# Kernel tuning notes

Hardware: AMD Instinct MI355X
Metric: run time of the kernel (lower is better)

## Reference

```python
import jax, jax.numpy as jnp
import numpy as np

K = 3          # kernel_size
PAD = 1        # padding
FOCAL = 50.0
DMIN = 1.0
DMAX = 50.0
ORIG_H = 512.0  # original_image_size[1]


def setup_inputs() -> dict:
    key = jax.random.key(0)
    k1, k2 = jax.random.split(key)
    x = jax.random.normal(k1, (4, 64, 256, 256), dtype=jnp.float32)
    # conv weight [out_ch, in_ch, K, K] (bias=False)
    W = jax.random.normal(k2, (64, 64, K, K), dtype=jnp.float32) * 0.05
    return {"x": x, "W": W}


def _bilinear(img, xs, ys):
    """Bilinear sample img [B,C,H,W] at float pixel coords xs, ys [B,Ho,Wo].
    Zero padding outside the image (grid_sample semantics)."""
    B, C, H, Wd = img.shape
    Ho, Wo = xs.shape[1], xs.shape[2]
    x0 = jnp.floor(xs); y0 = jnp.floor(ys)
    wx1 = xs - x0; wx0 = 1.0 - wx1
    wy1 = ys - y0; wy0 = 1.0 - wy1
    img_flat = img.reshape(B, C, H * Wd)

    def gat(ix, iy):
        ixi = ix.astype(jnp.int32); iyi = iy.astype(jnp.int32)
        valid = (ixi >= 0) & (ixi < Wd) & (iyi >= 0) & (iyi < H)
        idx = jnp.clip(iyi, 0, H - 1) * Wd + jnp.clip(ixi, 0, Wd - 1)
        v = jnp.take_along_axis(img_flat, idx.reshape(B, 1, Ho * Wo), axis=2)
        v = v.reshape(B, C, Ho, Wo)
        return v * valid[:, None].astype(img.dtype)

    return (gat(x0, y0) * (wx0 * wy0)[:, None]
            + gat(x0 + 1, y0) * (wx1 * wy0)[:, None]
            + gat(x0, y0 + 1) * (wx0 * wy1)[:, None]
            + gat(x0 + 1, y0 + 1) * (wx1 * wy1)[:, None])


def reference(x, W):
    B, C, H, Wd = x.shape
    downsample = ORIG_H / H  # 2.0 for H=256

    # upper branch: plain 3x3 conv, padding 1, no bias
    x_upper = jax.lax.conv_general_dilated(x, W, (1, 1), [(PAD, PAD), (PAD, PAD)])

    # geometry -> clamped depth (geometry_method='max', formulation='depth')
    depth = jnp.clip(jnp.max(x, axis=1), DMIN, DMAX)  # [B,H,W]

    # Frontal homography: Hom01 = I with [1,2] = focal/(downsample*depth);
    # its inverse Hom10 shifts y by -s.
    s = FOCAL / (downsample * depth)  # [B,H,W]

    xi = jnp.arange(Wd, dtype=x.dtype)[None, None, :]
    yi = jnp.arange(H, dtype=x.dtype)[None, :, None]
    xs = jnp.broadcast_to(xi, (B, H, Wd))
    ys = yi - s  # Hom10 applied to pixel coords

    # warp input with per-pixel Hom10 (pass_warped_images=True)
    x2 = _bilinear(x, xs, ys)

    # deformable conv: per-pixel offset from Hom10 is (dx,dy)=(0,-s) for all 9 taps
    x_lower = jnp.zeros_like(x_upper)
    for ky in range(K):
        for kx in range(K):
            sx = xs + (kx - PAD)
            sy = ys + (ky - PAD)
            tap = _bilinear(x2, sx, sy)  # [B,C,H,W]
            x_lower = x_lower + jnp.einsum('bchw,oc->bohw', tap, W[:, :, ky, kx])

    # project with 'min' over the stacked (upper, lower) branches
    return jnp.minimum(x_upper, x_lower)
```

## Files before the change

### kernel.cpp

```cpp
#include <hip/hip_runtime.h>
#include <cmath>

constexpr int BB = 4, CC = 64, HH = 256, WW = 256;
constexpr int WP = 258;
constexpr int C2R = 257;

typedef short short8 __attribute__((ext_vector_type(8)));
typedef float f32x4 __attribute__((ext_vector_type(4)));
#define MFMA_BF16 __builtin_amdgcn_mfma_f32_16x16x32_bf16

typedef __attribute__((address_space(1))) const unsigned gptr_t;
typedef __attribute__((address_space(3))) unsigned lptr_t;

union U16x8 { uint4 v; unsigned short h[8]; };
union U16x4 { uint2 v; unsigned short h[4]; };

__device__ inline unsigned short f2bf(float f) {
  unsigned u = __builtin_bit_cast(unsigned, f);
  u += 0x7fffu + ((u >> 16) & 1u);
  return (unsigned short)(u >> 16);
}
__device__ inline unsigned short f2bf_trunc(float f) {
  return (unsigned short)(__builtin_bit_cast(unsigned, f) >> 16);
}
__device__ inline float bf2f(unsigned short h) {
  unsigned u = ((unsigned)h) << 16;
  return __builtin_bit_cast(float, u);
}

__global__ __launch_bounds__(256, 4) void k_pack(const float* __restrict__ x,
                                                 const float* __restrict__ Wt,
                                                 float* __restrict__ s,
                                                 unsigned short* __restrict__ xn,
                                                 unsigned short* __restrict__ Wp) {
  __shared__ float tile[CC * 129];
  __shared__ float pmax[2][128];
  const int t = threadIdx.x;
  const int half = blockIdx.x & 1, y = blockIdx.x >> 1, b = blockIdx.y;
  const int px0 = half * 128;
  const int pxl = t & 127, chb = (t >> 7) * 32;

  if (b == 0 && blockIdx.x < 18) {
    int gid = blockIdx.x * 256 + t;
    int lane = gid & 63, kc = (gid >> 6) & 1, mt = (gid >> 7) & 3, tap = gid >> 9;
    int o = mt * 16 + (lane & 15);
    int kb = kc * 32 + (lane >> 4) * 8;
    int ky = tap / 3, kx = tap % 3;
    U16x8 r;
#pragma unroll
    for (int j = 0; j < 8; ++j)
      r.h[j] = f2bf(Wt[o * 576 + (kb + j) * 9 + ky * 3 + kx]);
    ((uint4*)Wp)[gid] = r.v;
  }

  const float* base = x + (size_t)b * CC * HH * WW + (size_t)y * WW + px0 + pxl;
  float m = -1e30f;
#pragma unroll 8
  for (int i = 0; i < 32; ++i) {
    float v = base[(size_t)(chb + i) * HH * WW];
    tile[(chb + i) * 129 + pxl] = v;
    m = fmaxf(m, v);
  }
  pmax[t >> 7][pxl] = m;

  uint4* xn4 = (uint4*)xn;
  if (t < 8) {
    int col = half ? (WP - 1) : 0;
    xn4[(((size_t)(b * HH + y) * WP + col) * CC + t * 8) >> 3] =
        make_uint4(0, 0, 0, 0);
  }
  __syncthreads();

  if (t < 128) {
    float mm = fmaxf(pmax[0][t], pmax[1][t]);
    s[(b * HH + y) * WW + px0 + t] = 25.0f / fminf(fmaxf(mm, 1.0f), 50.0f);
  }
#pragma unroll
  for (int g = 0; g < 4; ++g) {
    int px = g * 32 + (t >> 3), c8 = t & 7;
    U16x8 r;
#pragma unroll
    for (int j = 0; j < 8; ++j) r.h[j] = f2bf(tile[(c8 * 8 + j) * 129 + px]);
    xn4[(((size_t)(b * HH + y) * WP + px0 + px + 1) * CC + c8 * 8) >> 3] = r.v;
  }
}

__global__ __launch_bounds__(256, 4) void k_lower(const unsigned short* __restrict__ xn,
                                                  const unsigned short* __restrict__ Wp,
                                                  const float* __restrict__ s,
                                                  unsigned short* __restrict__ c2) {
  __shared__ uint4 lds[2112];
  const int t = threadIdx.x;
  const int ctile = blockIdx.x & 3, tr = blockIdx.x >> 2;
  const int b = blockIdx.y;
  const int r0 = tr * 2 - 1;
  const int colBase = ctile * 64;

  const uint4* xn4 = (const uint4*)xn;

  float sva[9];
#pragma unroll
  for (int j = 0; j < 9; ++j) {
    int idx = j * 256 + t;
    bool act = (j < 8) || (t < 64);
    int rr_ = idx / 528, rem = idx % 528;
    int col_ = rem >> 3;
    int xrow = r0 - 1 + rr_;
    bool va = act && (xrow >= 0) && (xrow < HH);
    int pxc = min(max(colBase + col_ - 1, 0), WW - 1);
    sva[j] = va ? s[(b * HH + min(max(xrow, 0), HH - 1)) * WW + pxc] : 0.0f;
  }

#pragma unroll
  for (int h = 0; h < 2; ++h) {
    const int jb = h * 5;
    const int n = h ? 4 : 5;
    uint4 u0[5], u1[5];
    float w0a[5], w1a[5];
    int la[5];
    bool act[5], va[5];
#pragma unroll
    for (int j = 0; j < 5; ++j) {
      if (j >= n) break;
      const int e = jb + j;
      int idx = e * 256 + t;
      act[j] = (e < 8) || (t < 64);
      int rr_ = idx / 528, rem = idx % 528;
      int col_ = rem >> 3, ch_ = rem & 7;
      int xrow = r0 - 1 + rr_;
      va[j] = act[j] && (xrow >= 0) && (xrow < HH);
      la[j] = (rr_ * 66 + col_) * 8 + (ch_ ^ (col_ & 7));
      float ys = (float)xrow - sva[e];
      float fy = floorf(ys);
      float wfr = ys - fy;
      int i0 = (int)fy;
      w0a[j] = (i0 >= 0) ? 1.0f - wfr : 0.0f;
      w1a[j] = (i0 + 1 >= 0) ? wfr : 0.0f;
      int a0 = min(max(i0, 0), HH - 1), a1 = min(max(i0 + 1, 0), HH - 1);
      int o0 = ((b * HH + a0) * WP + colBase + col_) * 8 + ch_;
      int o1 = ((b * HH + a1) * WP + colBase + col_) * 8 + ch_;
      if (va[j]) {
        u0[j] = xn4[o0];
        u1[j] = xn4[o1];
      }
    }
#pragma unroll
    for (int j = 0; j < 5; ++j) {
      if (j >= n) break;
      if (act[j]) {
        uint4 v = make_uint4(0, 0, 0, 0);
        if (va[j]) {
          U16x8 a, bb, rr;
          a.v = u0[j];
          bb.v = u1[j];
#pragma unroll
          for (int k = 0; k < 8; ++k)
            rr.h[k] = f2bf_trunc(w0a[j] * bf2f(a.h[k]) + w1a[j] * bf2f(bb.h[k]));
          v = rr.v;
        }
        lds[la[j]] = v;
      }
    }
  }

  const int lane = t & 63, w = t >> 6;
  const int ow = w & 1, ch2 = w >> 1;
  const int quad = lane >> 4, l15 = lane & 15;
  const uint4* wp4 = (const uint4*)Wp;
  __syncthreads();

  f32x4 acc[2][2][2];
#pragma unroll
  for (int pt = 0; pt < 2; ++pt)
#pragma unroll
    for (int rr = 0; rr < 2; ++rr)
#pragma unroll
      for (int ct = 0; ct < 2; ++ct) acc[pt][rr][ct] = {0.f, 0.f, 0.f, 0.f};

#pragma unroll 1
  for (int kc = 0; kc < 2; ++kc) {
    short8 wf[9][2];
#pragma unroll
    for (int tap = 0; tap < 9; ++tap)
#pragma unroll
      for (int ct = 0; ct < 2; ++ct)
        wf[tap][ct] = __builtin_bit_cast(
            short8, wp4[((tap * 4 + (ow * 2 + ct)) * 2 + kc) * 64 + lane]);
#pragma unroll
    for (int pt = 0; pt < 2; ++pt) {
#pragma unroll
      for (int ir = 0; ir < 4; ++ir) {
#pragma unroll
        for (int kx = 0; kx < 3; ++kx) {
          int col = ch2 * 32 + pt * 16 + l15 + kx;
          short8 xf = __builtin_bit_cast(
              short8, lds[(ir * 66 + col) * 8 + ((kc * 4 + quad) ^ (col & 7))]);
          if (ir <= 2) {
#pragma unroll
            for (int ct = 0; ct < 2; ++ct)
              acc[pt][0][ct] = MFMA_BF16(wf[ir * 3 + kx][ct], xf, acc[pt][0][ct], 0, 0, 0);
          }
          if (ir >= 1) {
#pragma unroll
            for (int ct = 0; ct < 2; ++ct)
              acc[pt][1][ct] = MFMA_BF16(wf[(ir - 1) * 3 + kx][ct], xf, acc[pt][1][ct], 0, 0, 0);
          }
        }
      }
    }
  }

  __syncthreads();
  uint2* sb = (uint2*)lds;
#pragma unroll
  for (int pt = 0; pt < 2; ++pt) {
    int pxl = ch2 * 32 + pt * 16 + l15;
#pragma unroll
    for (int rr = 0; rr < 2; ++rr) {
#pragma unroll
      for (int ct = 0; ct < 2; ++ct) {
        f32x4 A = acc[pt][rr][ct];
        int og = (ow * 2 + ct) * 4 + quad;
        unsigned short h0 = f2bf(A[0]), h1 = f2bf(A[1]), h2 = f2bf(A[2]), h3 = f2bf(A[3]);
        sb[(rr * 64 + pxl) * 18 + og] =
            make_uint2((unsigned)h0 | ((unsigned)h1 << 16),
                       (unsigned)h2 | ((unsigned)h3 << 16));
      }
    }
  }
  __syncthreads();
  {
    uint2* c2u = (uint2*)c2;
    int h = t & 1, u = t >> 1;
    int rr = u >> 6, pxl = u & 63;
    int r = r0 + rr;
    if (r < 256) {
      const uint2* srcp = sb + u * 18 + h * 8;
      uint4 q0 = *(const uint4*)(srcp + 0);
      uint4 q1 = *(const uint4*)(srcp + 2);
      uint4 q2 = *(const uint4*)(srcp + 4);
      uint4 q3 = *(const uint4*)(srcp + 6);
      uint4* dst = (uint4*)(c2u + ((((size_t)(b * C2R + (r + 1)) * WW) + colBase + pxl) << 4) + h * 8);
      dst[0] = q0; dst[1] = q1; dst[2] = q2; dst[3] = q3;
    }
  }
}

__global__ __launch_bounds__(256, 4) void k_final(const unsigned short* __restrict__ xn,
                                                  const unsigned short* __restrict__ Wp,
                                                  const float* __restrict__ s,
                                                  const unsigned short* __restrict__ c2,
                                                  float* __restrict__ out) {
  __shared__ uint4 lds[2112];
  const int t = threadIdx.x;
  const int ctile = blockIdx.x & 3, tr = blockIdx.x >> 2;
  const int b = blockIdx.y;
  const int y0 = tr * 2;
  const int colBase = ctile * 64;

  const int lane = t & 63, w = t >> 6;
  const int ow = w & 1, ch2 = w >> 1;
  const int quad = lane >> 4, l15 = lane & 15;
  const uint4* src4 = (const uint4*)xn;
  const uint4* wp4 = (const uint4*)Wp;

  float sv_e[2][2];
#pragma unroll
  for (int pt = 0; pt < 2; ++pt)
#pragma unroll
    for (int rr = 0; rr < 2; ++rr)
      sv_e[pt][rr] =
          s[(b * HH + (y0 + rr)) * WW + (colBase + ch2 * 32 + pt * 16 + l15)];

  if (tr > 0 && tr < 127) {
#pragma unroll
    for (int i = 0; i < 8; ++i) {
      int idx = i * 256 + t;
      int rr_ = idx / 528, rem = idx % 528;
      int col_ = rem >> 3, ch_ = rem & 7;
      int xrow = y0 - 1 + rr_;
      size_t srcIdx =
          ((size_t)(b * HH + xrow) * WP + colBase + col_) * 8 + (ch_ ^ (col_ & 7));
      __builtin_amdgcn_global_load_lds((gptr_t*)(const void*)(src4 + srcIdx),
                                       (lptr_t*)(void*)&lds[i * 256 + (t & 192)],
                                       16, 0, 0);
    }
    if (t < 64) {
      int idx = 2048 + t;
      int rr_ = idx / 528, rem = idx % 528;
      int col_ = rem >> 3, ch_ = rem & 7;
      int xrow = y0 - 1 + rr_;
      size_t srcIdx =
          ((size_t)(b * HH + xrow) * WP + colBase + col_) * 8 + (ch_ ^ (col_ & 7));
      __builtin_amdgcn_global_load_lds((gptr_t*)(const void*)(src4 + srcIdx),
                                       (lptr_t*)(void*)&lds[2048],
                                       16, 0, 0);
    }
  } else {
#pragma unroll
    for (int i = 0; i < 9; ++i) {
      int idx = i * 256 + t;
      if (idx < 2112) {
        int rr_ = idx / 528, rem = idx % 528;
        int col_ = rem >> 3, ch_ = rem & 7;
        int xrow = y0 - 1 + rr_;
        uint4 v = make_uint4(0, 0, 0, 0);
        if (xrow >= 0 && xrow < HH)
          v = src4[((size_t)(b * HH + xrow) * WP + colBase + col_) * 8 + ch_];
        lds[(rr_ * 66 + col_) * 8 + (ch_ ^ (col_ & 7))] = v;
      }
    }
  }
  __syncthreads();

  f32x4 acc[2][2][2];
#pragma unroll
  for (int pt = 0; pt < 2; ++pt)
#pragma unroll
    for (int rr = 0; rr < 2; ++rr)
#pragma unroll
      for (int ct = 0; ct < 2; ++ct) acc[pt][rr][ct] = {0.f, 0.f, 0.f, 0.f};

#pragma unroll 1
  for (int kc = 0; kc < 2; ++kc) {
    short8 wf[9][2];
#pragma unroll
    for (int tap = 0; tap < 9; ++tap)
#pragma unroll
      for (int ct = 0; ct < 2; ++ct)
        wf[tap][ct] = __builtin_bit_cast(
            short8, wp4[((tap * 4 + (ow * 2 + ct)) * 2 + kc) * 64 + lane]);
#pragma unroll
    for (int pt = 0; pt < 2; ++pt) {
#pragma unroll
      for (int ir = 0; ir < 4; ++ir) {
#pragma unroll
        for (int kx = 0; kx < 3; ++kx) {
          int col = ch2 * 32 + pt * 16 + l15 + kx;
          short8 xf = __builtin_bit_cast(
              short8, lds[(ir * 66 + col) * 8 + ((kc * 4 + quad) ^ (col & 7))]);
          if (ir <= 2) {
#pragma unroll
            for (int ct = 0; ct < 2; ++ct)
              acc[pt][0][ct] = MFMA_BF16(wf[ir * 3 + kx][ct], xf, acc[pt][0][ct], 0, 0, 0);
          }
          if (ir >= 1) {
#pragma unroll
            for (int ct = 0; ct < 2; ++ct)
              acc[pt][1][ct] = MFMA_BF16(wf[(ir - 1) * 3 + kx][ct], xf, acc[pt][1][ct], 0, 0, 0);
          }
        }
      }
    }
  }

  __syncthreads();
  float* lf = (float*)lds;
  const uint2* c2u = (const uint2*)c2;
#pragma unroll
  for (int pt = 0; pt < 2; ++pt) {
    int pxl = ch2 * 32 + pt * 16 + l15;
    int px = colBase + pxl;
#pragma unroll
    for (int rr = 0; rr < 2; ++rr) {
      int y = y0 + rr;
      float sv = sv_e[pt][rr];
      float ys = (float)y - sv;
      float fy = floorf(ys);
      float wfr = ys - fy;
      int i0 = (int)fy;
      float lw0 = (i0 + 1 >= 0 && i0 + 1 <= HH) ? 1.0f - wfr : 0.0f;
      float lw1 = (i0 + 2 >= 0 && i0 + 2 <= HH) ? wfr : 0.0f;
      int a0 = min(max(i0 + 1, 0), HH);
      int a1 = min(max(i0 + 2, 0), HH);
#pragma unroll
      for (int ct = 0; ct < 2; ++ct) {
        f32x4 A = acc[pt][rr][ct];
        int og = (ow * 2 + ct) * 4 + quad;
        U16x4 v0, v1;
        v0.v = c2u[(((size_t)(b * C2R + a0) * WW + px) << 4) + og];
        v1.v = c2u[(((size_t)(b * C2R + a1) * WW + px) << 4) + og];
#pragma unroll
        for (int reg = 0; reg < 4; ++reg) {
          float lower = lw0 * bf2f(v0.h[reg]) + lw1 * bf2f(v1.h[reg]);
          int u = rr * 64 + og * 4 + reg;
          lf[u * 64 + (((pxl >> 2) ^ (u & 15)) << 2) + (pxl & 3)] =
              fminf(A[reg], lower);
        }
      }
    }
  }
  __syncthreads();
#pragma unroll
  for (int j = 0; j < 8; ++j) {
    int u = w * 32 + j * 4 + (lane >> 4);
    int c = u & 63, rr = u >> 6;
    int lp = lane & 15;
    const float* srcp = lf + u * 64 + ((lp ^ (u & 15)) << 2);
    float4 q = *(const float4*)srcp;
    *(float4*)(out + ((size_t)(b * CC + c) * HH + (y0 + rr)) * WW + colBase +
               lp * 4) = q;
  }
}

extern "C" void kernel_launch(void* const* d_in, const int* in_sizes, int n_in,
                              void* d_out, int out_size, void* d_ws, size_t ws_size,
                              hipStream_t stream) {
  const float* x = (const float*)d_in[0];
  const float* Wt = (const float*)d_in[1];
  float* out = (float*)d_out;

  char* ws = (char*)d_ws;
  float* s = (float*)ws;
  unsigned short* Wp = (unsigned short*)(ws + 1048576);
  unsigned short* xn = (unsigned short*)(ws + 1122304);
  unsigned short* c2 = (unsigned short*)(ws + 34938880);
  k_pack<<<dim3(HH * 2, BB), 256, 0, stream>>>(x, Wt, s, xn, Wp);
  k_lower<<<dim3(4 * 129, BB), 256, 0, stream>>>(xn, Wp, s, c2);
  k_final<<<dim3(4 * 128, BB), 256, 0, stream>>>(xn, Wp, s, c2, out);
}
```

Measured before the change: 187.4 us.

## Merge lower and final conv kernels into one ticket-scheduled persistent-style launch

Combines the two conv kernels into a single launch in which blocks take an atomic ticket. Lower-branch tiles come first, and final tiles come after them. Each final tile computes its upper-branch conv before spin-waiting on a per-batch counter of completed lower tiles. This removes a kernel launch boundary and lets the final tiles' upper conv overlap the tail of the lower tiles. The cost is a global atomic per block, a spin-wait, and a dependency on forward progress of ticket ordering.

```diff
diff --git a/kernel.cpp b/kernel.cpp
--- a/kernel.cpp
+++ b/kernel.cpp
@@ -5,6 +5,11 @@
 constexpr int WP = 258;
 constexpr int C2R = 257;
 
+constexpr int NLOW = 516;
+constexpr int NFIN = 512;
+constexpr int TLOW = NLOW * BB;
+constexpr int TTOT = TLOW + NFIN * BB;
+
 typedef short short8 __attribute__((ext_vector_type(8)));
 typedef float f32x4 __attribute__((ext_vector_type(4)));
 #define MFMA_BF16 __builtin_amdgcn_mfma_f32_16x16x32_bf16
@@ -14,6 +19,9 @@
 
 union U16x8 { uint4 v; unsigned short h[8]; };
 union U16x4 { uint2 v; unsigned short h[4]; };
+
+__device__ unsigned g_ticket;
+__device__ unsigned g_cnt[BB];
 
 __device__ inline unsigned short f2bf(float f) {
   unsigned u = __builtin_bit_cast(unsigned, f);
@@ -40,6 +48,11 @@
   const int px0 = half * 128;
   const int pxl = t & 127, chb = (t >> 7) * 32;
 
+  if (blockIdx.x == 0 && b == 0) {
+    if (t == 0) g_ticket = 0;
+    else if (t <= BB) g_cnt[t - 1] = 0;
+  }
+
   if (b == 0 && blockIdx.x < 18) {
     int gid = blockIdx.x * 256 + t;
     int lane = gid & 63, kc = (gid >> 6) & 1, mt = (gid >> 7) & 3, tap = gid >> 9;
@@ -85,321 +98,332 @@
   }
 }
 
-__global__ __launch_bounds__(256, 4) void k_lower(const unsigned short* __restrict__ xn,
-                                                  const unsigned short* __restrict__ Wp,
-                                                  const float* __restrict__ s,
-                                                  unsigned short* __restrict__ c2) {
+__global__ __launch_bounds__(256, 4) void k_conv(const unsigned short* __restrict__ xn,
+                                                 const unsigned short* __restrict__ Wp,
+                                                 const float* __restrict__ s,
+                                                 unsigned short* __restrict__ c2,
+                                                 float* __restrict__ out) {
   __shared__ uint4 lds[2112];
+  __shared__ unsigned stick;
   const int t = threadIdx.x;
-  const int ctile = blockIdx.x & 3, tr = blockIdx.x >> 2;
-  const int b = blockIdx.y;
-  const int r0 = tr * 2 - 1;
-  const int colBase = ctile * 64;
-
-  const uint4* xn4 = (const uint4*)xn;
-
-  float sva[9];
-#pragma unroll
-  for (int j = 0; j < 9; ++j) {
-    int idx = j * 256 + t;
-    bool act = (j < 8) || (t < 64);
-    int rr_ = idx / 528, rem = idx % 528;
-    int col_ = rem >> 3;
-    int xrow = r0 - 1 + rr_;
-    bool va = act && (xrow >= 0) && (xrow < HH);
-    int pxc = min(max(colBase + col_ - 1, 0), WW - 1);
-    sva[j] = va ? s[(b * HH + min(max(xrow, 0), HH - 1)) * WW + pxc] : 0.0f;
-  }
-
-#pragma unroll
-  for (int h = 0; h < 2; ++h) {
-    const int jb = h * 5;
-    const int n = h ? 4 : 5;
-    uint4 u0[5], u1[5];
-    float w0a[5], w1a[5];
-    int la[5];
-    bool act[5], va[5];
-#pragma unroll
-    for (int j = 0; j < 5; ++j) {
-      if (j >= n) break;
-      const int e = jb + j;
-      int idx = e * 256 + t;
-      act[j] = (e < 8) || (t < 64);
-      int rr_ = idx / 528, rem = idx % 528;
-      int col_ = rem >> 3, ch_ = rem & 7;
-      int xrow = r0 - 1 + rr_;
-      va[j] = act[j] && (xrow >= 0) && (xrow < HH);
-      la[j] = (rr_ * 66 + col_) * 8 + (ch_ ^ (col_ & 7));
-      float ys = (float)xrow - sva[e];
-      float fy = floorf(ys);
-      float wfr = ys - fy;
-      int i0 = (int)fy;
-      w0a[j] = (i0 >= 0) ? 1.0f - wfr : 0.0f;
-      w1a[j] = (i0 + 1 >= 0) ? wfr : 0.0f;
-      int a0 = min(max(i0, 0), HH - 1), a1 = min(max(i0 + 1, 0), HH - 1);
-      int o0 = ((b * HH + a0) * WP + colBase + col_) * 8 + ch_;
-      int o1 = ((b * HH + a1) * WP + colBase + col_) * 8 + ch_;
-      if (va[j]) {
-        u0[j] = xn4[o0];
-        u1[j] = xn4[o1];
-      }
-    }
-#pragma unroll
-    for (int j = 0; j < 5; ++j) {
-      if (j >= n) break;
-      if (act[j]) {
-        uint4 v = make_uint4(0, 0, 0, 0);
-        if (va[j]) {
-          U16x8 a, bb, rr;
-          a.v = u0[j];
-          bb.v = u1[j];
-#pragma unroll
-          for (int k = 0; k < 8; ++k)
-            rr.h[k] = f2bf_trunc(w0a[j] * bf2f(a.h[k]) + w1a[j] * bf2f(bb.h[k]));
-          v = rr.v;
-        }
-        lds[la[j]] = v;
-      }
-    }
-  }
+  if (t == 0) stick = atomicAdd(&g_ticket, 1u) % TTOT;
+  __syncthreads();
+  const unsigned ticket = stick;
 
   const int lane = t & 63, w = t >> 6;
   const int ow = w & 1, ch2 = w >> 1;
   const int quad = lane >> 4, l15 = lane & 15;
   const uint4* wp4 = (const uint4*)Wp;
-  __syncthreads();
-
-  f32x4 acc[2][2][2];
-#pragma unroll
-  for (int pt = 0; pt < 2; ++pt)
-#pragma unroll
-    for (int rr = 0; rr < 2; ++rr)
-#pragma unroll
-      for (int ct = 0; ct < 2; ++ct) acc[pt][rr][ct] = {0.f, 0.f, 0.f, 0.f};
+  const uint4* xn4 = (const uint4*)xn;
+
+  if (ticket < TLOW) {
+    const int b = ticket / NLOW;
+    const int rem = ticket % NLOW;
+    const int ctile = rem & 3, tr = rem >> 2;
+    const int r0 = tr * 2 - 1;
+    const int colBase = ctile * 64;
+
+    float sva[9];
+#pragma unroll
+    for (int j = 0; j < 9; ++j) {
+      int idx = j * 256 + t;
+      bool act = (j < 8) || (t < 64);
+      int rr_ = idx / 528, rem2 = idx % 528;
+      int col_ = rem2 >> 3;
+      int xrow = r0 - 1 + rr_;
+      bool va = act && (xrow >= 0) && (xrow < HH);
+      int pxc = min(max(colBase + col_ - 1, 0), WW - 1);
+      sva[j] = va ? s[(b * HH + min(max(xrow, 0), HH - 1)) * WW + pxc] : 0.0f;
+    }
+
+#pragma unroll
+    for (int h = 0; h < 2; ++h) {
+      const int jb = h * 5;
+      const int n = h ? 4 : 5;
+      uint4 u0[5], u1[5];
+      float w0a[5], w1a[5];
+      int la[5];
+      bool act[5], va[5];
+#pragma unroll
+      for (int j = 0; j < 5; ++j) {
+        if (j >= n) break;
+        const int e = jb + j;
+        int idx = e * 256 + t;
+        act[j] = (e < 8) || (t < 64);
+        int rr_ = idx / 528, rem2 = idx % 528;
+        int col_ = rem2 >> 3, ch_ = rem2 & 7;
+        int xrow = r0 - 1 + rr_;
+        va[j] = act[j] && (xrow >= 0) && (xrow < HH);
+        la[j] = (rr_ * 66 + col_) * 8 + (ch_ ^ (col_ & 7));
+        float ys = (float)xrow - sva[e];
+        float fy = floorf(ys);
+        float wfr = ys - fy;
+        int i0 = (int)fy;
+        w0a[j] = (i0 >= 0) ? 1.0f - wfr : 0.0f;
+        w1a[j] = (i0 + 1 >= 0) ? wfr : 0.0f;
+        int a0 = min(max(i0, 0), HH - 1), a1 = min(max(i0 + 1, 0), HH - 1);
+        int o0 = ((b * HH + a0) * WP + colBase + col_) * 8 + ch_;
+        int o1 = ((b * HH + a1) * WP + colBase + col_) * 8 + ch_;
+        if (va[j]) {
+          u0[j] = xn4[o0];
+          u1[j] = xn4[o1];
+        }
+      }
+#pragma unroll
+      for (int j = 0; j < 5; ++j) {
+        if (j >= n) break;
+        if (act[j]) {
+          uint4 v = make_uint4(0, 0, 0, 0);
+          if (va[j]) {
+            U16x8 a, bb, rr;
+            a.v = u0[j];
+            bb.v = u1[j];
+#pragma unroll
+            for (int k = 0; k < 8; ++k)
+              rr.h[k] = f2bf_trunc(w0a[j] * bf2f(a.h[k]) + w1a[j] * bf2f(bb.h[k]));
+            v = rr.v;
+          }
+          lds[la[j]] = v;
+        }
+      }
+    }
+    __syncthreads();
+
+    f32x4 acc[2][2][2];
+#pragma unroll
+    for (int pt = 0; pt < 2; ++pt)
+#pragma unroll
+      for (int rr = 0; rr < 2; ++rr)
+#pragma unroll
+        for (int ct = 0; ct < 2; ++ct) acc[pt][rr][ct] = {0.f, 0.f, 0.f, 0.f};
 
 #pragma unroll 1
-  for (int kc = 0; kc < 2; ++kc) {
-    short8 wf[9][2];
-#pragma unroll
-    for (int tap = 0; tap < 9; ++tap)
-#pragma unroll
-      for (int ct = 0; ct < 2; ++ct)
-        wf[tap][ct] = __builtin_bit_cast(
-            short8, wp4[((tap * 4 + (ow * 2 + ct)) * 2 + kc) * 64 + lane]);
+    for (int kc = 0; kc < 2; ++kc) {
+      short8 wf[9][2];
+#pragma unroll
+      for (int tap = 0; tap < 9; ++tap)
+#pragma unroll
+        for (int ct = 0; ct < 2; ++ct)
+          wf[tap][ct] = __builtin_bit_cast(
+              short8, wp4[((tap * 4 + (ow * 2 + ct)) * 2 + kc) * 64 + lane]);
+#pragma unroll
+      for (int pt = 0; pt < 2; ++pt) {
+#pragma unroll
+        for (int ir = 0; ir < 4; ++ir) {
+#pragma unroll
+          for (int kx = 0; kx < 3; ++kx) {
+            int col = ch2 * 32 + pt * 16 + l15 + kx;
+            short8 xf = __builtin_bit_cast(
+                short8, lds[(ir * 66 + col) * 8 + ((kc * 4 + quad) ^ (col & 7))]);
+            if (ir <= 2) {
+#pragma unroll
+              for (int ct = 0; ct < 2; ++ct)
+                acc[pt][0][ct] = MFMA_BF16(wf[ir * 3 + kx][ct], xf, acc[pt][0][ct], 0, 0, 0);
+            }
+            if (ir >= 1) {
+#pragma unroll
+              for (int ct = 0; ct < 2; ++ct)
+                acc[pt][1][ct] = MFMA_BF16(wf[(ir - 1) * 3 + kx][ct], xf, acc[pt][1][ct], 0, 0, 0);
+            }
+          }
+        }
+      }
+    }
+
+    __syncthreads();
+    uint2* sb = (uint2*)lds;
 #pragma unroll
     for (int pt = 0; pt < 2; ++pt) {
-#pragma unroll
-      for (int ir = 0; ir < 4; ++ir) {
-#pragma unroll
-        for (int kx = 0; kx < 3; ++kx) {
-          int col = ch2 * 32 + pt * 16 + l15 + kx;
-          short8 xf = __builtin_bit_cast(
-              short8, lds[(ir * 66 + col) * 8 + ((kc * 4 + quad) ^ (col & 7))]);
-          if (ir <= 2) {
-#pragma unroll
-            for (int ct = 0; ct < 2; ++ct)
-              acc[pt][0][ct] = MFMA_BF16(wf[ir * 3 + kx][ct], xf, acc[pt][0][ct], 0, 0, 0);
+      int pxl = ch2 * 32 + pt * 16 + l15;
+#pragma unroll
+      for (int rr = 0; rr < 2; ++rr) {
+#pragma unroll
+        for (int ct = 0; ct < 2; ++ct) {
+          f32x4 A = acc[pt][rr][ct];
+          int og = (ow * 2 + ct) * 4 + quad;
+          unsigned short h0 = f2bf(A[0]), h1 = f2bf(A[1]), h2 = f2bf(A[2]), h3 = f2bf(A[3]);
+          sb[(rr * 64 + pxl) * 18 + og] =
+              make_uint2((unsigned)h0 | ((unsigned)h1 << 16),
+                         (unsigned)h2 | ((unsigned)h3 << 16));
+        }
+      }
+    }
+    __syncthreads();
+    {
+      uint2* c2u = (uint2*)c2;
+      int h = t & 1, u = t >> 1;
+      int rr = u >> 6, pxl = u & 63;
+      int r = r0 + rr;
+      if (r < 256) {
+        const uint2* srcp = sb + u * 18 + h * 8;
+        uint4 q0 = *(const uint4*)(srcp + 0);
+        uint4 q1 = *(const uint4*)(srcp + 2);
+        uint4 q2 = *(const uint4*)(srcp + 4);
+        uint4 q3 = *(const uint4*)(srcp + 6);
+        uint4* dst = (uint4*)(c2u + ((((size_t)(b * C2R + (r + 1)) * WW) + colBase + pxl) << 4) + h * 8);
+        dst[0] = q0; dst[1] = q1; dst[2] = q2; dst[3] = q3;
+      }
+    }
+
+    __syncthreads();
+    if (t == 0) {
+      __threadfence();
+      atomicAdd(&g_cnt[b], 1u);
+    }
+
+  } else {
+    const unsigned f = ticket - TLOW;
+    const int b = f / NFIN;
+    const int rem = f % NFIN;
+    const int ctile = rem & 3, tr = rem >> 2;
+    const int y0 = tr * 2;
+    const int colBase = ctile * 64;
+    const uint4* src4 = xn4;
+
+    float sv_e[2][2];
+#pragma unroll
+    for (int pt = 0; pt < 2; ++pt)
+#pragma unroll
+      for (int rr = 0; rr < 2; ++rr)
+        sv_e[pt][rr] =
+            s[(b * HH + (y0 + rr)) * WW + (colBase + ch2 * 32 + pt * 16 + l15)];
+
+    if (tr > 0 && tr < 127) {
+#pragma unroll
+      for (int i = 0; i < 8; ++i) {
+        int idx = i * 256 + t;
+        int rr_ = idx / 528, rem2 = idx % 528;
+        int col_ = rem2 >> 3, ch_ = rem2 & 7;
+        int xrow = y0 - 1 + rr_;
+        size_t srcIdx =
+            ((size_t)(b * HH + xrow) * WP + colBase + col_) * 8 + (ch_ ^ (col_ & 7));
+        __builtin_amdgcn_global_load_lds((gptr_t*)(const void*)(src4 + srcIdx),
+                                         (lptr_t*)(void*)&lds[i * 256 + (t & 192)],
+                                         16, 0, 0);
+      }
+      if (t < 64) {
+        int idx = 2048 + t;
+        int rr_ = idx / 528, rem2 = idx % 528;
+        int col_ = rem2 >> 3, ch_ = rem2 & 7;
+        int xrow = y0 - 1 + rr_;
+        size_t srcIdx =
+            ((size_t)(b * HH + xrow) * WP + colBase + col_) * 8 + (ch_ ^ (col_ & 7));
+        __builtin_amdgcn_global_load_lds((gptr_t*)(const void*)(src4 + srcIdx),
+                                         (lptr_t*)(void*)&lds[2048],
+                                         16, 0, 0);
+      }
+    } else {
+#pragma unroll
+      for (int i = 0; i < 9; ++i) {
+        int idx = i * 256 + t;
+        if (idx < 2112) {
+          int rr_ = idx / 528, rem2 = idx % 528;
+          int col_ = rem2 >> 3, ch_ = rem2 & 7;
+          int xrow = y0 - 1 + rr_;
+          uint4 v = make_uint4(0, 0, 0, 0);
+          if (xrow >= 0 && xrow < HH)
+            v = src4[((size_t)(b * HH + xrow) * WP + colBase + col_) * 8 + ch_];
+          lds[(rr_ * 66 + col_) * 8 + (ch_ ^ (col_ & 7))] = v;
+        }
+      }
+    }
+    __syncthreads();
+
+    f32x4 acc[2][2][2];
+#pragma unroll
+    for (int pt = 0; pt < 2; ++pt)
+#pragma unroll
+      for (int rr = 0; rr < 2; ++rr)
+#pragma unroll
+        for (int ct = 0; ct < 2; ++ct) acc[pt][rr][ct] = {0.f, 0.f, 0.f, 0.f};
+
+#pragma unroll 1
+    for (int kc = 0; kc < 2; ++kc) {
+      short8 wf[9][2];
+#pragma unroll
+      for (int tap = 0; tap < 9; ++tap)
+#pragma unroll
+        for (int ct = 0; ct < 2; ++ct)
+          wf[tap][ct] = __builtin_bit_cast(
+              short8, wp4[((tap * 4 + (ow * 2 + ct)) * 2 + kc) * 64 + lane]);
+#pragma unroll
+      for (int pt = 0; pt < 2; ++pt) {
+#pragma unroll
+        for (int ir = 0; ir < 4; ++ir) {
+#pragma unroll
+          for (int kx = 0; kx < 3; ++kx) {
+            int col = ch2 * 32 + pt * 16 + l15 + kx;
+            short8 xf = __builtin_bit_cast(
+                short8, lds[(ir * 66 + col) * 8 + ((kc * 4 + quad) ^ (col & 7))]);
+            if (ir <= 2) {
+#pragma unroll
+              for (int ct = 0; ct < 2; ++ct)
+                acc[pt][0][ct] = MFMA_BF16(wf[ir * 3 + kx][ct], xf, acc[pt][0][ct], 0, 0, 0);
+            }
+            if (ir >= 1) {
+#pragma unroll
+              for (int ct = 0; ct < 2; ++ct)
+                acc[pt][1][ct] = MFMA_BF16(wf[(ir - 1) * 3 + kx][ct], xf, acc[pt][1][ct], 0, 0, 0);
+            }
           }
-          if (ir >= 1) {
-#pragma unroll
-            for (int ct = 0; ct < 2; ++ct)
-              acc[pt][1][ct] = MFMA_BF16(wf[(ir - 1) * 3 + kx][ct], xf, acc[pt][1][ct], 0, 0, 0);
+        }
+      }
+    }
+
+    if (t == 0) {
+      while (__hip_atomic_load(&g_cnt[b], __ATOMIC_RELAXED,
+                               __HIP_MEMORY_SCOPE_AGENT) < (unsigned)NLOW)
+        __builtin_amdgcn_s_sleep(32);
+      __threadfence();
+    }
+    __syncthreads();
+
+    float* lf = (float*)lds;
+    const uint2* c2u = (const uint2*)c2;
+#pragma unroll
+    for (int pt = 0; pt < 2; ++pt) {
+      int pxl = ch2 * 32 + pt * 16 + l15;
+      int px = colBase + pxl;
+#pragma unroll
+      for (int rr = 0; rr < 2; ++rr) {
+        int y = y0 + rr;
+        float sv = sv_e[pt][rr];
+        float ys = (float)y - sv;
+        float fy = floorf(ys);
+        float wfr = ys - fy;
+        int i0 = (int)fy;
+        float lw0 = (i0 + 1 >= 0 && i0 + 1 <= HH) ? 1.0f - wfr : 0.0f;
+        float lw1 = (i0 + 2 >= 0 && i0 + 2 <= HH) ? wfr : 0.0f;
+        int a0 = min(max(i0 + 1, 0), HH);
+        int a1 = min(max(i0 + 2, 0), HH);
+#pragma unroll
+        for (int ct = 0; ct < 2; ++ct) {
+          f32x4 A = acc[pt][rr][ct];
+          int og = (ow * 2 + ct) * 4 + quad;
+          U16x4 v0, v1;
+          v0.v = c2u[(((size_t)(b * C2R + a0) * WW + px) << 4) + og];
+          v1.v = c2u[(((size_t)(b * C2R + a1) * WW + px) << 4) + og];
+#pragma unroll
+          for (int reg = 0; reg < 4; ++reg) {
+            float lower = lw0 * bf2f(v0.h[reg]) + lw1 * bf2f(v1.h[reg]);
+            int u = rr * 64 + og * 4 + reg;
+            lf[u * 64 + (((pxl >> 2) ^ (u & 15)) << 2) + (pxl & 3)] =
+                fminf(A[reg], lower);
           }
         }
       }
     }
-  }
-
-  __syncthreads();
-  uint2* sb = (uint2*)lds;
-#pragma unroll
-  for (int pt = 0; pt < 2; ++pt) {
-    int pxl = ch2 * 32 + pt * 16 + l15;
-#pragma unroll
-    for (int rr = 0; rr < 2; ++rr) {
-#pragma unroll
-      for (int ct = 0; ct < 2; ++ct) {
-        f32x4 A = acc[pt][rr][ct];
-        int og = (ow * 2 + ct) * 4 + quad;
-        unsigned short h0 = f2bf(A[0]), h1 = f2bf(A[1]), h2 = f2bf(A[2]), h3 = f2bf(A[3]);
-        sb[(rr * 64 + pxl) * 18 + og] =
-            make_uint2((unsigned)h0 | ((unsigned)h1 << 16),
-                       (unsigned)h2 | ((unsigned)h3 << 16));
-      }
-    }
-  }
-  __syncthreads();
-  {
-    uint2* c2u = (uint2*)c2;
-    int h = t & 1, u = t >> 1;
-    int rr = u >> 6, pxl = u & 63;
-    int r = r0 + rr;
-    if (r < 256) {
-      const uint2* srcp = sb + u * 18 + h * 8;
-      uint4 q0 = *(const uint4*)(srcp + 0);
-      uint4 q1 = *(const uint4*)(srcp + 2);
-      uint4 q2 = *(const uint4*)(srcp + 4);
-      uint4 q3 = *(const uint4*)(srcp + 6);
-      uint4* dst = (uint4*)(c2u + ((((size_t)(b * C2R + (r + 1)) * WW) + colBase + pxl) << 4) + h * 8);
-      dst[0] = q0; dst[1] = q1; dst[2] = q2; dst[3] = q3;
-    }
-  }
-}
-
-__global__ __launch_bounds__(256, 4) void k_final(const unsigned short* __restrict__ xn,
-                                                  const unsigned short* __restrict__ Wp,
-                                                  const float* __restrict__ s,
-                                                  const unsigned short* __restrict__ c2,
-                                                  float* __restrict__ out) {
-  __shared__ uint4 lds[2112];
-  const int t = threadIdx.x;
-  const int ctile = blockIdx.x & 3, tr = blockIdx.x >> 2;
-  const int b = blockIdx.y;
-  const int y0 = tr * 2;
-  const int colBase = ctile * 64;
-
-  const int lane = t & 63, w = t >> 6;
-  const int ow = w & 1, ch2 = w >> 1;
-  const int quad = lane >> 4, l15 = lane & 15;
-  const uint4* src4 = (const uint4*)xn;
-  const uint4* wp4 = (const uint4*)Wp;
-
-  float sv_e[2][2];
-#pragma unroll
-  for (int pt = 0; pt < 2; ++pt)
-#pragma unroll
-    for (int rr = 0; rr < 2; ++rr)
-      sv_e[pt][rr] =
-          s[(b * HH + (y0 + rr)) * WW + (colBase + ch2 * 32 + pt * 16 + l15)];
-
-  if (tr > 0 && tr < 127) {
-#pragma unroll
-    for (int i = 0; i < 8; ++i) {
-      int idx = i * 256 + t;
-      int rr_ = idx / 528, rem = idx % 528;
-      int col_ = rem >> 3, ch_ = rem & 7;
-      int xrow = y0 - 1 + rr_;
-      size_t srcIdx =
-          ((size_t)(b * HH + xrow) * WP + colBase + col_) * 8 + (ch_ ^ (col_ & 7));
-      __builtin_amdgcn_global_load_lds((gptr_t*)(const void*)(src4 + srcIdx),
-                                       (lptr_t*)(void*)&lds[i * 256 + (t & 192)],
-                                       16, 0, 0);
-    }
-    if (t < 64) {
-      int idx = 2048 + t;
-      int rr_ = idx / 528, rem = idx % 528;
-      int col_ = rem >> 3, ch_ = rem & 7;
-      int xrow = y0 - 1 + rr_;
-      size_t srcIdx =
-          ((size_t)(b * HH + xrow) * WP + colBase + col_) * 8 + (ch_ ^ (col_ & 7));
-      __builtin_amdgcn_global_load_lds((gptr_t*)(const void*)(src4 + srcIdx),
-                                       (lptr_t*)(void*)&lds[2048],
-                                       16, 0, 0);
-    }
-  } else {
-#pragma unroll
-    for (int i = 0; i < 9; ++i) {
-      int idx = i * 256 + t;
-      if (idx < 2112) {
-        int rr_ = idx / 528, rem = idx % 528;
-        int col_ = rem >> 3, ch_ = rem & 7;
-        int xrow = y0 - 1 + rr_;
-        uint4 v = make_uint4(0, 0, 0, 0);
-        if (xrow >= 0 && xrow < HH)
-          v = src4[((size_t)(b * HH + xrow) * WP + colBase + col_) * 8 + ch_];
-        lds[(rr_ * 66 + col_) * 8 + (ch_ ^ (col_ & 7))] = v;
-      }
-    }
-  }
-  __syncthreads();
-
-  f32x4 acc[2][2][2];
-#pragma unroll
-  for (int pt = 0; pt < 2; ++pt)
-#pragma unroll
-    for (int rr = 0; rr < 2; ++rr)
-#pragma unroll
-      for (int ct = 0; ct < 2; ++ct) acc[pt][rr][ct] = {0.f, 0.f, 0.f, 0.f};
-
-#pragma unroll 1
-  for (int kc = 0; kc < 2; ++kc) {
-    short8 wf[9][2];
-#pragma unroll
-    for (int tap = 0; tap < 9; ++tap)
-#pragma unroll
-      for (int ct = 0; ct < 2; ++ct)
-        wf[tap][ct] = __builtin_bit_cast(
-            short8, wp4[((tap * 4 + (ow * 2 + ct)) * 2 + kc) * 64 + lane]);
-#pragma unroll
-    for (int pt = 0; pt < 2; ++pt) {
-#pragma unroll
-      for (int ir = 0; ir < 4; ++ir) {
-#pragma unroll
-        for (int kx = 0; kx < 3; ++kx) {
-          int col = ch2 * 32 + pt * 16 + l15 + kx;
-          short8 xf = __builtin_bit_cast(
-              short8, lds[(ir * 66 + col) * 8 + ((kc * 4 + quad) ^ (col & 7))]);
-          if (ir <= 2) {
-#pragma unroll
-            for (int ct = 0; ct < 2; ++ct)
-              acc[pt][0][ct] = MFMA_BF16(wf[ir * 3 + kx][ct], xf, acc[pt][0][ct], 0, 0, 0);
-          }
-          if (ir >= 1) {
-#pragma unroll
-            for (int ct = 0; ct < 2; ++ct)
-              acc[pt][1][ct] = MFMA_BF16(wf[(ir - 1) * 3 + kx][ct], xf, acc[pt][1][ct], 0, 0, 0);
-          }
-        }
-      }
-    }
-  }
-
-  __syncthreads();
-  float* lf = (float*)lds;
-  const uint2* c2u = (const uint2*)c2;
-#pragma unroll
-  for (int pt = 0; pt < 2; ++pt) {
-    int pxl = ch2 * 32 + pt * 16 + l15;
-    int px = colBase + pxl;
-#pragma unroll
-    for (int rr = 0; rr < 2; ++rr) {
-      int y = y0 + rr;
-      float sv = sv_e[pt][rr];
-      float ys = (float)y - sv;
-      float fy = floorf(ys);
-      float wfr = ys - fy;
-      int i0 = (int)fy;
-      float lw0 = (i0 + 1 >= 0 && i0 + 1 <= HH) ? 1.0f - wfr : 0.0f;
-      float lw1 = (i0 + 2 >= 0 && i0 + 2 <= HH) ? wfr : 0.0f;
-      int a0 = min(max(i0 + 1, 0), HH);
-      int a1 = min(max(i0 + 2, 0), HH);
-#pragma unroll
-      for (int ct = 0; ct < 2; ++ct) {
-        f32x4 A = acc[pt][rr][ct];
-        int og = (ow * 2 + ct) * 4 + quad;
-        U16x4 v0, v1;
-        v0.v = c2u[(((size_t)(b * C2R + a0) * WW + px) << 4) + og];
-        v1.v = c2u[(((size_t)(b * C2R + a1) * WW + px) << 4) + og];
-#pragma unroll
-        for (int reg = 0; reg < 4; ++reg) {
-          float lower = lw0 * bf2f(v0.h[reg]) + lw1 * bf2f(v1.h[reg]);
-          int u = rr * 64 + og * 4 + reg;
-          lf[u * 64 + (((pxl >> 2) ^ (u & 15)) << 2) + (pxl & 3)] =
-              fminf(A[reg], lower);
-        }
-      }
-    }
-  }
-  __syncthreads();
-#pragma unroll
-  for (int j = 0; j < 8; ++j) {
-    int u = w * 32 + j * 4 + (lane >> 4);
-    int c = u & 63, rr = u >> 6;
-    int lp = lane & 15;
-    const float* srcp = lf + u * 64 + ((lp ^ (u & 15)) << 2);
-    float4 q = *(const float4*)srcp;
-    *(float4*)(out + ((size_t)(b * CC + c) * HH + (y0 + rr)) * WW + colBase +
-               lp * 4) = q;
+    __syncthreads();
+#pragma unroll
+    for (int j = 0; j < 8; ++j) {
+      int u = w * 32 + j * 4 + (lane >> 4);
+      int c = u & 63, rr = u >> 6;
+      int lp = lane & 15;
+      const float* srcp = lf + u * 64 + ((lp ^ (u & 15)) << 2);
+      float4 q = *(const float4*)srcp;
+      *(float4*)(out + ((size_t)(b * CC + c) * HH + (y0 + rr)) * WW + colBase +
+                 lp * 4) = q;
+    }
   }
 }
 
@@ -416,6 +440,5 @@
   unsigned short* xn = (unsigned short*)(ws + 1122304);
   unsigned short* c2 = (unsigned short*)(ws + 34938880);
   k_pack<<<dim3(HH * 2, BB), 256, 0, stream>>>(x, Wt, s, xn, Wp);
-  k_lower<<<dim3(4 * 129, BB), 256, 0, stream>>>(xn, Wp, s, c2);
-  k_final<<<dim3(4 * 128, BB), 256, 0, stream>>>(xn, Wp, s, c2, out);
-}
+  k_conv<<<dim3(TTOT), 256, 0, stream>>>(xn, Wp, s, c2, out);
+}
```

Result: slower. 411.0 us (+119.4%).
